# Performance work log

Hardware: AMD Instinct MI355X
Metric: run time of the kernel (lower is better)

Reference implementation:

```python
import jax, jax.numpy as jnp
import numpy as np

B, T, D, H, L = 8, 150, 30, 5, 3
HD = D // H  # 6
ORIG = (300, 74, 35)


def setup_inputs() -> dict:
    key = jax.random.key(0)
    ks = iter(jax.random.split(key, 40))
    def g(shape, s=0.05):
        return jax.random.normal(next(ks), shape, dtype=jnp.float32) * s
    return {
        "x_l": g((B, T, ORIG[0]), 1.0),
        "x_a": g((B, T, ORIG[1]), 1.0),
        "x_v": g((B, T, ORIG[2]), 1.0),
        "Wl": g((D, ORIG[0])),
        "Wa": g((D, ORIG[1])),
        "Wv": g((D, ORIG[2])),
        "in_w": g((2, L, 3 * D, D)),
        "in_b": jnp.zeros((2, L, 3 * D), jnp.float32),
        "out_w": g((2, L, D, D)),
        "out_b": jnp.zeros((2, L, D), jnp.float32),
        "lin1_w": g((2, L, 4 * D, D)),
        "lin1_b": jnp.zeros((2, L, 4 * D), jnp.float32),
        "lin2_w": g((2, L, D, 4 * D)),
        "lin2_b": jnp.zeros((2, L, D), jnp.float32),
        "n1_g": jnp.ones((2, L, D), jnp.float32),
        "n1_b": jnp.zeros((2, L, D), jnp.float32),
        "n2_g": jnp.ones((2, L, D), jnp.float32),
        "n2_b": jnp.zeros((2, L, D), jnp.float32),
        "p1_w": g((2 * D, 2 * D)),
        "p1_b": jnp.zeros((2 * D,), jnp.float32),
        "p2_w": g((2 * D, 2 * D)),
        "p2_b": jnp.zeros((2 * D,), jnp.float32),
        "ow": g((1, 2 * D)),
        "ob": jnp.zeros((1,), jnp.float32),
    }


def _ln(x, g, b, eps=1e-5):
    m = x.mean(-1, keepdims=True)
    v = jnp.var(x, axis=-1, keepdims=True)  # biased var, matches torch LayerNorm
    return (x - m) * jax.lax.rsqrt(v + eps) * g + b


def _heads(x):  # [Tt, B, D] -> [B*H, Tt, HD]
    Tt = x.shape[0]
    return x.reshape(Tt, B * H, HD).transpose(1, 0, 2)


def _layer(x, xk, xv, p):
    iw, ib, ow, ob, w1, b1, w2, b2, g1, bb1, g2, bb2 = p
    res = x
    xn, kn, vn = _ln(x, g1, bb1), _ln(xk, g1, bb1), _ln(xv, g1, bb1)
    q = (xn @ iw[:D].T + ib[:D]) * (HD ** -0.5)
    k = kn @ iw[D:2 * D].T + ib[D:2 * D]
    v = vn @ iw[2 * D:].T + ib[2 * D:]
    qh, kh, vh = _heads(q), _heads(k), _heads(v)
    # trilinear scores: [B*H, Tq, Tk, Tv]
    aw = jnp.einsum('iat,ibt,ict->iabc', qh, kh, vh)
    fused = aw.mean(-1) + aw.max(-1)          # fuse over value axis -> [B*H, Tq, Tk]
    fused = jax.nn.softmax(fused, axis=-1)
    attn = jnp.einsum('iab,ibt->iat', fused, qh)  # NB: original bmm uses q, not v
    attn = attn.transpose(1, 0, 2).reshape(-1, B, D)
    x = res + (attn @ ow.T + ob)
    res = x
    xn = _ln(x, g2, bb2)
    x = jax.nn.relu(xn @ w1.T + b1) @ w2.T + b2
    return res + x


def reference(x_l, x_a, x_v, Wl, Wa, Wv, in_w, in_b, out_w, out_b,
              lin1_w, lin1_b, lin2_w, lin2_b, n1_g, n1_b, n2_g, n2_b,
              p1_w, p1_b, p2_w, p2_b, ow, ob):
    pl = (x_l @ Wl.T).transpose(1, 0, 2)  # [T, B, D] (conv1d k=1, no bias)
    pa = (x_a @ Wa.T).transpose(1, 0, 2)
    pv = (x_v @ Wv.T).transpose(1, 0, 2)
    hs = []
    for s, (kk, vv) in enumerate(((pa, pv), (pv, pa))):
        h = pl
        for l in range(L):
            p = (in_w[s, l], in_b[s, l], out_w[s, l], out_b[s, l],
                 lin1_w[s, l], lin1_b[s, l], lin2_w[s, l], lin2_b[s, l],
                 n1_g[s, l], n1_b[s, l], n2_g[s, l], n2_b[s, l])
            h = _layer(h, kk, vv, p)
        hs.append(h[-1])  # last timestep [B, D]
    last_hs = jnp.concatenate(hs, axis=1)  # [B, 2D]
    proj = jax.nn.relu(last_hs @ p1_w.T + p1_b) @ p2_w.T + p2_b + last_hs
    out = proj @ ow.T + ob
    return (out, last_hs)
```

## Files before the change

kernel.cpp:

```cpp
#include <hip/hip_runtime.h>
#include <math.h>

#define BB 8
#define TT 150
#define DD 30
#define HH 5
#define HD 6
#define LL 3
#define NI 40
#define ROWF (TT*BB*DD)
#define RSTR 8
#define NR 152

typedef _Float16 half8 __attribute__((ext_vector_type(8)));
typedef float f32x16 __attribute__((ext_vector_type(16)));

__device__ __forceinline__ float wsum(float v) {
    #pragma unroll
    for (int m = 32; m > 0; m >>= 1) v += __shfl_xor(v, m, 64);
    return v;
}

__global__ __launch_bounds__(256) void proj3_kernel(
    const float* __restrict__ x_l, const float* __restrict__ x_a, const float* __restrict__ x_v,
    const float* __restrict__ Wl, const float* __restrict__ Wa, const float* __restrict__ Wv,
    float* __restrict__ pl, float* __restrict__ pa, float* __restrict__ pv) {
    int blk = blockIdx.x;
    int which = blk / 300;
    int w = threadIdx.x >> 6, lane = threadIdx.x & 63;
    int rowu = (blk % 300) * 4 + w;
    int t = rowu / BB, b = rowu % BB;
    const float* x = which == 0 ? x_l : (which == 1 ? x_a : x_v);
    const float* W = which == 0 ? Wl : (which == 1 ? Wa : Wv);
    float* out = which == 0 ? pl : (which == 1 ? pa : pv);
    int Cin = which == 0 ? 300 : (which == 1 ? 74 : 35);
    int cst = Cin | 1;
    __shared__ float WS[30 * 301];
    __shared__ float xr[4][304];
    for (int j = threadIdx.x; j < DD * Cin; j += 256)
        WS[(j / Cin) * cst + (j % Cin)] = W[j];
    const float* xp = x + ((size_t)b * TT + t) * Cin;
    for (int j = lane; j < Cin; j += 64) xr[w][j] = xp[j];
    __syncthreads();
    int d = lane >> 1, jh = lane & 1;
    int h1 = Cin >> 1;
    int j0 = jh ? h1 : 0, j1 = jh ? Cin : h1;
    const float* wr = WS + (size_t)(d < DD ? d : 0) * cst;
    float acc = 0.f;
    for (int j = j0; j < j1; j++) acc += xr[w][j] * wr[j];
    acc += __shfl_xor(acc, 1, 64);
    if (jh == 0 && d < DD) out[t * (BB * DD) + b * DD + d] = acc;
}

__global__ __launch_bounds__(256) void kvq0_kernel(
    const float* __restrict__ pl, const float* __restrict__ pa, const float* __restrict__ pv,
    const float* __restrict__ in_w, const float* __restrict__ in_b,
    const float* __restrict__ n1g, const float* __restrict__ n1b,
    _Float16* __restrict__ k_all, _Float16* __restrict__ v_all, _Float16* __restrict__ q) {
    int blk = blockIdx.x;
    int w = threadIdx.x >> 6, lane = threadIdx.x & 63;
    __shared__ float iwS[1800];
    __shared__ float xn[4][2][30];
    if (blk < 1800) {
        int po = blk / 300;
        int s = po / LL;
        int tb = (blk % 300) * 4 + w;
        int t = tb / BB, b = tb % BB;
        const float* xk = (s == 0) ? pa : pv;
        const float* xv = (s == 0) ? pv : pa;
        const float* iw = in_w + (size_t)po * 2700 + 900;
        const float* ib = in_b + (size_t)po * 90;
        const float* g  = n1g + (size_t)po * 30;
        const float* bb = n1b + (size_t)po * 30;
        for (int j = threadIdx.x; j < 1800; j += 256) iwS[j] = iw[j];
        const float* rows[2] = { xk + (size_t)tb * 30, xv + (size_t)tb * 30 };
        for (int r = 0; r < 2; r++) {
            float xval = (lane < 30) ? rows[r][lane] : 0.f;
            float mean = wsum(xval) * (1.f / 30.f);
            float dv = (lane < 30) ? (xval - mean) : 0.f;
            float var = wsum(dv * dv) * (1.f / 30.f);
            float inv = rsqrtf(var + 1e-5f);
            if (lane < 30) xn[w][r][lane] = dv * inv * g[lane] + bb[lane];
        }
        __syncthreads();
        if (lane < 60) {
            int which = lane / 30, dd = lane % 30;
            const float* wr = iwS + lane * 30;
            const float* xv2 = xn[w][which];
            float acc = 0.f;
            #pragma unroll 6
            for (int j = 0; j < 30; j++) acc += wr[j] * xv2[j];
            acc += ib[30 + lane];
            int i = b * HH + dd / HD, hd = dd % HD;
            _Float16* dst = which ? v_all : k_all;
            size_t row = (((size_t)po * NI + i) * TT + t) * 8;
            dst[row + hd] = (_Float16)acc;
            if (hd < 2) dst[row + 6 + hd] = (_Float16)0.f;
        }
    } else {
        int r2 = blk - 1800;
        int s = r2 / 300;
        int tb = (r2 % 300) * 4 + w;
        int t = tb / BB, b = tb % BB;
        int po = s * LL;
        const float* iw = in_w + (size_t)po * 2700;
        const float* ib = in_b + (size_t)po * 90;
        const float* g  = n1g + (size_t)po * 30;
        const float* bb = n1b + (size_t)po * 30;
        for (int j = threadIdx.x; j < 900; j += 256) iwS[j] = iw[j];
        const float* row = pl + (size_t)tb * 30;
        float xval = (lane < 30) ? row[lane] : 0.f;
        float mean = wsum(xval) * (1.f / 30.f);
        float dv = (lane < 30) ? (xval - mean) : 0.f;
        float var = wsum(dv * dv) * (1.f / 30.f);
        float inv = rsqrtf(var + 1e-5f);
        if (lane < 30) xn[w][0][lane] = dv * inv * g[lane] + bb[lane];
        __syncthreads();
        if (lane < 30) {
            const float* wr = iwS + lane * 30;
            float acc = 0.f;
            #pragma unroll 6
            for (int j = 0; j < 30; j++) acc += wr[j] * xn[w][0][j];
            acc = (acc + ib[lane]) * 0.40824829046386307f;
            int i = b * HH + lane / HD, hd = lane % HD;
            size_t rw = (((size_t)s * NI + i) * TT + t) * 8;
            q[rw + hd] = (_Float16)acc;
            if (hd < 2) q[rw + 6 + hd] = (_Float16)0.f;
        }
    }
}

__global__ __launch_bounds__(256, 4) void score_kernel(
    const _Float16* __restrict__ q, const _Float16* __restrict__ k_all,
    const _Float16* __restrict__ v_all, int l, float* __restrict__ attn) {
    int blk = blockIdx.x;
    int s = blk / 760;
    int rem = blk % 760;
    int i = rem / 19;
    int g = rem % 19;
    int tid = threadIdx.x;
    int wv = tid >> 6, lane = tid & 63;
    int lo = lane & 31, hf = lane >> 5;
    int po = s * LL + l;

    __shared__ __align__(16) _Float16 qsh[NR * RSTR];
    __shared__ __align__(16) _Float16 ksh[NR * RSTR];
    __shared__ __align__(16) _Float16 vsh[NR * RSTR];

    const _Float16* qg = q + (size_t)(s * NI + i) * TT * 8;
    const _Float16* kg = k_all + ((size_t)po * NI + i) * TT * 8;
    const _Float16* vg = v_all + ((size_t)po * NI + i) * TT * 8;
    half8 z8;
    #pragma unroll
    for (int t = 0; t < 8; t++) z8[t] = (_Float16)0.f;
    for (int r = tid; r < NR; r += 256) {
        half8 qa = z8, ka = z8, va = z8;
        if (r < TT) {
            qa = *(const half8*)&qg[r * 8];
            ka = *(const half8*)&kg[r * 8];
            va = *(const half8*)&vg[r * 8];
        }
        *(half8*)&qsh[r * RSTR] = qa;
        *(half8*)&ksh[r * RSTR] = ka;
        *(half8*)&vsh[r * RSTR] = va;
    }
    __syncthreads();
    if (wv == 0) {
        float v6[6] = {0.f, 0.f, 0.f, 0.f, 0.f, 0.f};
        for (int c = lane; c < TT; c += 64) {
            #pragma unroll
            for (int t = 0; t < 6; t++) v6[t] += (float)vsh[c * RSTR + t];
        }
        #pragma unroll
        for (int m = 32; m > 0; m >>= 1) {
            #pragma unroll
            for (int t = 0; t < 6; t++) v6[t] += __shfl_xor(v6[t], m, 64);
        }
        if (lane < 6) vsh[TT * RSTR + lane] = (_Float16)(v6[lane] * (1.f / TT));
    }
    __syncthreads();

    f32x16 zacc;
    #pragma unroll
    for (int j = 0; j < 16; j++) zacc[j] = 0.f;

    half8 bfrag[5], vhalf[5];
    #pragma unroll
    for (int nt = 0; nt < 5; nt++) {
        int rr = nt * 32 + lo;
        int rc = rr < 151 ? rr : 151;
        half8 kf = *(const half8*)&ksh[rc * RSTR];
        half8 vf = *(const half8*)&vsh[rc * RSTR];
        bfrag[nt] = hf ? z8 : kf;
        vhalf[nt] = hf ? z8 : vf;
    }

    for (int ap = 0; ap < 2; ap++) {
        int a = g * 8 + wv * 2 + ap;
        if (a >= TT) break;
        half8 qav = *(const half8*)&qsh[a * RSTR];
        half8 afrag[5];
        #pragma unroll
        for (int nt = 0; nt < 5; nt++) afrag[nt] = vhalf[nt] * qav;

        float fsc[5];
        #pragma unroll
        for (int nb = 0; nb < 5; nb++) {
            float tm[4];
            #pragma unroll
            for (int ma = 0; ma < 4; ma++) {
                f32x16 acc = __builtin_amdgcn_mfma_f32_32x32x16_f16(afrag[ma], bfrag[nb], zacc, 0, 0, 0);
                float p0 = fmaxf(acc[0], acc[1]);
                float p1 = fmaxf(acc[2], acc[3]);
                float p2 = fmaxf(acc[4], acc[5]);
                float p3 = fmaxf(acc[6], acc[7]);
                float p4 = fmaxf(acc[8], acc[9]);
                float p5 = fmaxf(acc[10], acc[11]);
                float p6 = fmaxf(acc[12], acc[13]);
                float p7 = fmaxf(acc[14], acc[15]);
                float q0 = fmaxf(p0, p1), q1 = fmaxf(p2, p3);
                float q2 = fmaxf(p4, p5), q3 = fmaxf(p6, p7);
                tm[ma] = fmaxf(fmaxf(q0, q1), fmaxf(q2, q3));
            }
            f32x16 a4 = __builtin_amdgcn_mfma_f32_32x32x16_f16(afrag[4], bfrag[nb], zacc, 0, 0, 0);
            float s0 = fmaxf(a4[0], a4[1]);
            float s1 = fmaxf(a4[2], a4[3]);
            float s2 = fmaxf(a4[4], a4[5]);
            float s3 = fmaxf(a4[6], a4[7]);
            float s4 = fmaxf(a4[8], a4[9]);
            float ext = (hf == 0) ? fmaxf(a4[10], a4[11]) : -INFINITY;
            float m4 = fmaxf(fmaxf(fmaxf(s0, s1), fmaxf(s2, s3)), fmaxf(s4, ext));
            float rm = fmaxf(fmaxf(fmaxf(tm[0], tm[1]), fmaxf(tm[2], tm[3])), m4);
            float om = __shfl_xor(a4[10], 32, 64);
            float mn = hf ? a4[10] : om;
            rm = fmaxf(rm, __shfl_xor(rm, 32, 64));
            int bcol = nb * 32 + lo;
            fsc[nb] = (bcol < TT) ? (mn + rm) : -INFINITY;
        }
        float m = fmaxf(fmaxf(fsc[0], fsc[1]), fmaxf(fsc[2], fmaxf(fsc[3], fsc[4])));
        #pragma unroll
        for (int msk = 16; msk > 0; msk >>= 1) m = fmaxf(m, __shfl_xor(m, msk, 64));
        float e[5], es = 0.f;
        #pragma unroll
        for (int nb = 0; nb < 5; nb++) { e[nb] = __expf(fsc[nb] - m); es += e[nb]; }
        #pragma unroll
        for (int msk = 16; msk > 0; msk >>= 1) es += __shfl_xor(es, msk, 64);
        float acc6[6] = {0.f, 0.f, 0.f, 0.f, 0.f, 0.f};
        #pragma unroll
        for (int nb = 0; nb < 5; nb++) {
            int bcol = nb * 32 + lo;
            int bi = (bcol < TT) ? bcol : 0;
            float wgt = e[nb];
            half8 qrow = *(const half8*)&qsh[bi * RSTR];
            #pragma unroll
            for (int t = 0; t < 6; t++) acc6[t] += wgt * (float)qrow[t];
        }
        #pragma unroll
        for (int msk = 16; msk > 0; msk >>= 1) {
            #pragma unroll
            for (int t = 0; t < 6; t++) acc6[t] += __shfl_xor(acc6[t], msk, 64);
        }
        if (lane == 0) {
            float inv = 1.f / es;
            int bo = i / HH, ho = i % HH;
            float* dst = attn + (size_t)s * ROWF + a * (BB * DD) + bo * DD + ho * HD;
            #pragma unroll
            for (int t = 0; t < 6; t++) dst[t] = acc6[t] * inv;
        }
    }
}

__global__ __launch_bounds__(256) void ffnlnq_kernel(
    const float* __restrict__ attn, const float* __restrict__ pl,
    const float* __restrict__ out_w, const float* __restrict__ out_b,
    const float* __restrict__ l1w, const float* __restrict__ l1b,
    const float* __restrict__ l2w, const float* __restrict__ l2b,
    const float* __restrict__ n2g, const float* __restrict__ n2b,
    const float* __restrict__ in_w, const float* __restrict__ in_b,
    const float* __restrict__ n1g, const float* __restrict__ n1b,
    int l, int has_next,
    float* __restrict__ h, _Float16* __restrict__ q) {
    int blk = blockIdx.x;
    int s = blk / 300;
    int w = threadIdx.x >> 6, lane = threadIdx.x & 63;
    int tb = (blk % 300) * 4 + w;
    int t = tb / BB, b = tb % BB;
    int po = s * LL + l;
    const float* ow = out_w + (size_t)po * 900;
    const float* ob = out_b + (size_t)po * 30;
    const float* w1 = l1w + (size_t)po * 3600;
    const float* b1 = l1b + (size_t)po * 120;
    const float* w2 = l2w + (size_t)po * 3600;
    const float* b2 = l2b + (size_t)po * 30;
    const float* g2 = n2g + (size_t)po * 30;
    const float* bb2 = n2b + (size_t)po * 30;
    __shared__ float owS[900];
    __shared__ float w1T[30 * 128];
    __shared__ float w2S[30 * 121];
    __shared__ float iwqS[900];
    __shared__ float arS[4][30], xnS[4][32], hidS[4][120], xqS[4][30];
    for (int j = threadIdx.x; j < 900; j += 256) owS[j] = ow[j];
    for (int j = threadIdx.x; j < 3600; j += 256) w1T[(j % 30) * 128 + (j / 30)] = w1[j];
    for (int j = threadIdx.x; j < 3600; j += 256) w2S[(j / 120) * 121 + (j % 120)] = w2[j];
    if (has_next) {
        const float* iwq = in_w + (size_t)(po + 1) * 2700;
        for (int j = threadIdx.x; j < 900; j += 256) iwqS[j] = iwq[j];
    }
    __syncthreads();
    float* hrow = h + (size_t)s * ROWF + (size_t)tb * 30;
    const float* res = (l == 0) ? (pl + (size_t)tb * 30) : hrow;
    const float* arow = attn + (size_t)s * ROWF + (size_t)tb * 30;
    if (lane < 30) arS[w][lane] = arow[lane];
    float x1v = 0.f;
    if (lane < 30) {
        const float* wr = owS + lane * 30;
        float acc = 0.f;
        #pragma unroll 6
        for (int j = 0; j < 30; j++) acc += wr[j] * arS[w][j];
        x1v = res[lane] + acc + ob[lane];
    }
    float mean = wsum(x1v) * (1.f / 30.f);
    float dv = (lane < 30) ? (x1v - mean) : 0.f;
    float var = wsum(dv * dv) * (1.f / 30.f);
    float inv = rsqrtf(var + 1e-5f);
    if (lane < 30) xnS[w][lane] = dv * inv * g2[lane] + bb2[lane];
    for (int o = lane; o < 120; o += 64) {
        float acc = 0.f;
        #pragma unroll 6
        for (int j = 0; j < 30; j++) acc += w1T[j * 128 + o] * xnS[w][j];
        hidS[w][o] = fmaxf(acc + b1[o], 0.f);
    }
    float newh = 0.f;
    if (lane < 30) {
        const float* wr = w2S + lane * 121;
        float acc = 0.f;
        #pragma unroll 8
        for (int j = 0; j < 120; j++) acc += wr[j] * hidS[w][j];
        newh = x1v + acc + b2[lane];
        hrow[lane] = newh;
    }
    if (has_next) {
        const float* g1 = n1g + (size_t)(po + 1) * 30;
        const float* bb1 = n1b + (size_t)(po + 1) * 30;
        const float* ibq = in_b + (size_t)(po + 1) * 90;
        float mean2 = wsum(newh) * (1.f / 30.f);
        float dv2 = (lane < 30) ? (newh - mean2) : 0.f;
        float var2 = wsum(dv2 * dv2) * (1.f / 30.f);
        float inv2 = rsqrtf(var2 + 1e-5f);
        if (lane < 30) xqS[w][lane] = dv2 * inv2 * g1[lane] + bb1[lane];
        if (lane < 30) {
            const float* wr = iwqS + lane * 30;
            float acc = 0.f;
            #pragma unroll 6
            for (int j = 0; j < 30; j++) acc += wr[j] * xqS[w][j];
            acc = (acc + ibq[lane]) * 0.40824829046386307f;
            int i = b * HH + lane / HD, hd = lane % HD;
            size_t rw = (((size_t)s * NI + i) * TT + t) * 8;
            q[rw + hd] = (_Float16)acc;
            if (hd < 2) q[rw + 6 + hd] = (_Float16)0.f;
        }
    }
}

__global__ __launch_bounds__(256) void head_kernel(
    const float* __restrict__ h,
    const float* __restrict__ p1w, const float* __restrict__ p1b,
    const float* __restrict__ p2w, const float* __restrict__ p2b,
    const float* __restrict__ ow, const float* __restrict__ ob,
    float* __restrict__ out) {
    int tid = threadIdx.x;
    __shared__ float lh[480], hid[480], pr[480];
    for (int idx = tid; idx < 480; idx += 256) {
        int b = idx / 60, j = idx % 60;
        int s = j / 30, d = j % 30;
        float vv = h[(size_t)s * ROWF + 149 * (BB * DD) + b * DD + d];
        lh[idx] = vv;
        out[8 + idx] = vv;
    }
    __syncthreads();
    for (int idx = tid; idx < 480; idx += 256) {
        int b = idx / 60, o = idx % 60;
        const float* wr = p1w + o * 60;
        float acc = p1b[o];
        for (int j = 0; j < 60; j++) acc += wr[j] * lh[b * 60 + j];
        hid[idx] = fmaxf(acc, 0.f);
    }
    __syncthreads();
    for (int idx = tid; idx < 480; idx += 256) {
        int b = idx / 60, d = idx % 60;
        const float* wr = p2w + d * 60;
        float acc = p2b[d];
        for (int j = 0; j < 60; j++) acc += wr[j] * hid[b * 60 + j];
        pr[idx] = acc + lh[idx];
    }
    __syncthreads();
    if (tid < 8) {
        float acc = ob[0];
        for (int j = 0; j < 60; j++) acc += pr[tid * 60 + j] * ow[j];
        out[tid] = acc;
    }
}

extern "C" void kernel_launch(void* const* d_in, const int* in_sizes, int n_in,
                              void* d_out, int out_size, void* d_ws, size_t ws_size,
                              hipStream_t stream) {
    const float* x_l   = (const float*)d_in[0];
    const float* x_a   = (const float*)d_in[1];
    const float* x_v   = (const float*)d_in[2];
    const float* Wl    = (const float*)d_in[3];
    const float* Wa    = (const float*)d_in[4];
    const float* Wv    = (const float*)d_in[5];
    const float* in_w  = (const float*)d_in[6];
    const float* in_b  = (const float*)d_in[7];
    const float* out_w = (const float*)d_in[8];
    const float* out_b = (const float*)d_in[9];
    const float* l1w   = (const float*)d_in[10];
    const float* l1b   = (const float*)d_in[11];
    const float* l2w   = (const float*)d_in[12];
    const float* l2b   = (const float*)d_in[13];
    const float* n1g   = (const float*)d_in[14];
    const float* n1b   = (const float*)d_in[15];
    const float* n2g   = (const float*)d_in[16];
    const float* n2b   = (const float*)d_in[17];
    const float* p1w   = (const float*)d_in[18];
    const float* p1b   = (const float*)d_in[19];
    const float* p2w   = (const float*)d_in[20];
    const float* p2b   = (const float*)d_in[21];
    const float* oww   = (const float*)d_in[22];
    const float* obb   = (const float*)d_in[23];

    float* ws = (float*)d_ws;
    float* pl    = ws;
    float* pa    = ws + 36000;
    float* pv    = ws + 72000;
    float* h     = ws + 108000;
    float* at    = ws + 180000;
    _Float16* qh = (_Float16*)(ws + 252000);
    _Float16* kh = (_Float16*)(ws + 300000);
    _Float16* vh = (_Float16*)(ws + 444000);

    proj3_kernel<<<900, 256, 0, stream>>>(x_l, x_a, x_v, Wl, Wa, Wv, pl, pa, pv);
    kvq0_kernel<<<2400, 256, 0, stream>>>(pl, pa, pv, in_w, in_b, n1g, n1b,
                                          kh, vh, qh);
    for (int l = 0; l < LL; l++) {
        score_kernel<<<1520, 256, 0, stream>>>(qh, kh, vh, l, at);
        ffnlnq_kernel<<<600, 256, 0, stream>>>(at, pl, out_w, out_b, l1w, l1b, l2w, l2b,
                                               n2g, n2b, in_w, in_b, n1g, n1b,
                                               l, (l < LL - 1) ? 1 : 0, h, qh);
    }
    head_kernel<<<1, 256, 0, stream>>>(h, p1w, p1b, p2w, p2b, oww, obb, (float*)d_out);
}
```

Baseline: 247.9 us.

## Fuse input projection with K/V/Q prep and give score blocks more query rows

Merges the three modality projections and the layer-0 K/V/Q LayerNorm+projection into one kernel. Each (t,b) row is projected once, its normalization statistics are computed once and reused across all six parameter sets, and the pa/pv intermediate buffers are removed. Weights are now read straight from global memory instead of being staged in shared memory. Separately, the score kernel has each wave handle four query rows instead of two, halving the grid so the K/V staging is amortized over more work, at the cost of fewer blocks and less parallelism.

```diff
diff --git a/kernel.cpp b/kernel.cpp
--- a/kernel.cpp
+++ b/kernel.cpp
@@ -21,112 +21,126 @@
     return v;
 }
 
-__global__ __launch_bounds__(256) void proj3_kernel(
+__global__ __launch_bounds__(256) void projkvq_kernel(
     const float* __restrict__ x_l, const float* __restrict__ x_a, const float* __restrict__ x_v,
     const float* __restrict__ Wl, const float* __restrict__ Wa, const float* __restrict__ Wv,
-    float* __restrict__ pl, float* __restrict__ pa, float* __restrict__ pv) {
-    int blk = blockIdx.x;
-    int which = blk / 300;
-    int w = threadIdx.x >> 6, lane = threadIdx.x & 63;
-    int rowu = (blk % 300) * 4 + w;
-    int t = rowu / BB, b = rowu % BB;
-    const float* x = which == 0 ? x_l : (which == 1 ? x_a : x_v);
-    const float* W = which == 0 ? Wl : (which == 1 ? Wa : Wv);
-    float* out = which == 0 ? pl : (which == 1 ? pa : pv);
-    int Cin = which == 0 ? 300 : (which == 1 ? 74 : 35);
-    int cst = Cin | 1;
-    __shared__ float WS[30 * 301];
-    __shared__ float xr[4][304];
-    for (int j = threadIdx.x; j < DD * Cin; j += 256)
-        WS[(j / Cin) * cst + (j % Cin)] = W[j];
-    const float* xp = x + ((size_t)b * TT + t) * Cin;
-    for (int j = lane; j < Cin; j += 64) xr[w][j] = xp[j];
-    __syncthreads();
-    int d = lane >> 1, jh = lane & 1;
-    int h1 = Cin >> 1;
-    int j0 = jh ? h1 : 0, j1 = jh ? Cin : h1;
-    const float* wr = WS + (size_t)(d < DD ? d : 0) * cst;
-    float acc = 0.f;
-    for (int j = j0; j < j1; j++) acc += xr[w][j] * wr[j];
-    acc += __shfl_xor(acc, 1, 64);
-    if (jh == 0 && d < DD) out[t * (BB * DD) + b * DD + d] = acc;
-}
-
-__global__ __launch_bounds__(256) void kvq0_kernel(
-    const float* __restrict__ pl, const float* __restrict__ pa, const float* __restrict__ pv,
     const float* __restrict__ in_w, const float* __restrict__ in_b,
     const float* __restrict__ n1g, const float* __restrict__ n1b,
+    float* __restrict__ pl,
     _Float16* __restrict__ k_all, _Float16* __restrict__ v_all, _Float16* __restrict__ q) {
     int blk = blockIdx.x;
     int w = threadIdx.x >> 6, lane = threadIdx.x & 63;
-    __shared__ float iwS[1800];
-    __shared__ float xn[4][2][30];
-    if (blk < 1800) {
-        int po = blk / 300;
+    int tb = blk * 4 + w;
+    int t = tb / BB, b = tb % BB;
+
+    __shared__ float xl[4][304];
+    __shared__ float xa[4][80];
+    __shared__ float xv[4][40];
+    __shared__ float rrow[3][4][32];
+    __shared__ float dco[4][3][32];
+    __shared__ float xkv[4][2][32];
+    __shared__ float xq[4][32];
+
+    const float* xpl = x_l + ((size_t)b * TT + t) * 300;
+    const float* xpa = x_a + ((size_t)b * TT + t) * 74;
+    const float* xpv = x_v + ((size_t)b * TT + t) * 35;
+    for (int j = lane; j < 300; j += 64) xl[w][j] = xpl[j];
+    for (int j = lane; j < 74; j += 64) xa[w][j] = xpa[j];
+    if (lane < 35) xv[w][lane] = xpv[lane];
+    __syncthreads();
+
+    int d = lane >> 1, jh = lane & 1;
+    int dc = d < DD ? d : 0;
+    float accL, accA, accV;
+    {
+        const float* wr = Wl + (size_t)dc * 300;
+        int j0 = jh ? 150 : 0, j1 = jh ? 300 : 150;
+        float acc = 0.f;
+        for (int j = j0; j < j1; j++) acc += xl[w][j] * wr[j];
+        acc += __shfl_xor(acc, 1, 64);
+        accL = acc;
+    }
+    {
+        const float* wr = Wa + (size_t)dc * 74;
+        int j0 = jh ? 37 : 0, j1 = jh ? 74 : 37;
+        float acc = 0.f;
+        for (int j = j0; j < j1; j++) acc += xa[w][j] * wr[j];
+        acc += __shfl_xor(acc, 1, 64);
+        accA = acc;
+    }
+    {
+        const float* wr = Wv + (size_t)dc * 35;
+        int j0 = jh ? 17 : 0, j1 = jh ? 35 : 17;
+        float acc = 0.f;
+        for (int j = j0; j < j1; j++) acc += xv[w][j] * wr[j];
+        acc += __shfl_xor(acc, 1, 64);
+        accV = acc;
+    }
+    if (jh == 0 && d < DD) {
+        pl[t * (BB * DD) + b * DD + d] = accL;
+        rrow[0][w][d] = accL;
+        rrow[1][w][d] = accA;
+        rrow[2][w][d] = accV;
+    }
+    __syncthreads();
+
+    #pragma unroll
+    for (int src = 0; src < 3; src++) {
+        float xval = (lane < 30) ? rrow[src][w][lane] : 0.f;
+        float mean = wsum(xval) * (1.f / 30.f);
+        float dv = (lane < 30) ? (xval - mean) : 0.f;
+        float var = wsum(dv * dv) * (1.f / 30.f);
+        float inv = rsqrtf(var + 1e-5f);
+        if (lane < 30) dco[w][src][lane] = dv * inv;
+    }
+    __syncthreads();
+
+    for (int po = 0; po < 6; po++) {
         int s = po / LL;
-        int tb = (blk % 300) * 4 + w;
-        int t = tb / BB, b = tb % BB;
-        const float* xk = (s == 0) ? pa : pv;
-        const float* xv = (s == 0) ? pv : pa;
-        const float* iw = in_w + (size_t)po * 2700 + 900;
-        const float* ib = in_b + (size_t)po * 90;
-        const float* g  = n1g + (size_t)po * 30;
+        int kin = (s == 0) ? 1 : 2;
+        int vin = (s == 0) ? 2 : 1;
+        const float* g = n1g + (size_t)po * 30;
         const float* bb = n1b + (size_t)po * 30;
-        for (int j = threadIdx.x; j < 1800; j += 256) iwS[j] = iw[j];
-        const float* rows[2] = { xk + (size_t)tb * 30, xv + (size_t)tb * 30 };
-        for (int r = 0; r < 2; r++) {
-            float xval = (lane < 30) ? rows[r][lane] : 0.f;
-            float mean = wsum(xval) * (1.f / 30.f);
-            float dv = (lane < 30) ? (xval - mean) : 0.f;
-            float var = wsum(dv * dv) * (1.f / 30.f);
-            float inv = rsqrtf(var + 1e-5f);
-            if (lane < 30) xn[w][r][lane] = dv * inv * g[lane] + bb[lane];
+        int half = lane >> 5, dd2 = lane & 31;
+        if (dd2 < 30) {
+            int sel = half ? vin : kin;
+            xkv[w][half][dd2] = dco[w][sel][dd2] * g[dd2] + bb[dd2];
         }
         __syncthreads();
         if (lane < 60) {
             int which = lane / 30, dd = lane % 30;
-            const float* wr = iwS + lane * 30;
-            const float* xv2 = xn[w][which];
+            const float* wr = in_w + (size_t)po * 2700 + 900 + lane * 30;
             float acc = 0.f;
             #pragma unroll 6
-            for (int j = 0; j < 30; j++) acc += wr[j] * xv2[j];
-            acc += ib[30 + lane];
+            for (int j = 0; j < 30; j++) acc += wr[j] * xkv[w][which][j];
+            acc += in_b[po * 90 + 30 + lane];
             int i = b * HH + dd / HD, hd = dd % HD;
             _Float16* dst = which ? v_all : k_all;
             size_t row = (((size_t)po * NI + i) * TT + t) * 8;
             dst[row + hd] = (_Float16)acc;
             if (hd < 2) dst[row + 6 + hd] = (_Float16)0.f;
         }
-    } else {
-        int r2 = blk - 1800;
-        int s = r2 / 300;
-        int tb = (r2 % 300) * 4 + w;
-        int t = tb / BB, b = tb % BB;
-        int po = s * LL;
-        const float* iw = in_w + (size_t)po * 2700;
-        const float* ib = in_b + (size_t)po * 90;
-        const float* g  = n1g + (size_t)po * 30;
+        __syncthreads();
+    }
+
+    for (int s2 = 0; s2 < 2; s2++) {
+        int po = s2 * LL;
+        const float* g = n1g + (size_t)po * 30;
         const float* bb = n1b + (size_t)po * 30;
-        for (int j = threadIdx.x; j < 900; j += 256) iwS[j] = iw[j];
-        const float* row = pl + (size_t)tb * 30;
-        float xval = (lane < 30) ? row[lane] : 0.f;
-        float mean = wsum(xval) * (1.f / 30.f);
-        float dv = (lane < 30) ? (xval - mean) : 0.f;
-        float var = wsum(dv * dv) * (1.f / 30.f);
-        float inv = rsqrtf(var + 1e-5f);
-        if (lane < 30) xn[w][0][lane] = dv * inv * g[lane] + bb[lane];
+        if (lane < 30) xq[w][lane] = dco[w][0][lane] * g[lane] + bb[lane];
         __syncthreads();
         if (lane < 30) {
-            const float* wr = iwS + lane * 30;
+            const float* wr = in_w + (size_t)po * 2700 + lane * 30;
             float acc = 0.f;
             #pragma unroll 6
-            for (int j = 0; j < 30; j++) acc += wr[j] * xn[w][0][j];
-            acc = (acc + ib[lane]) * 0.40824829046386307f;
+            for (int j = 0; j < 30; j++) acc += wr[j] * xq[w][j];
+            acc = (acc + in_b[po * 90 + lane]) * 0.40824829046386307f;
             int i = b * HH + lane / HD, hd = lane % HD;
-            size_t rw = (((size_t)s * NI + i) * TT + t) * 8;
+            size_t rw = (((size_t)s2 * NI + i) * TT + t) * 8;
             q[rw + hd] = (_Float16)acc;
             if (hd < 2) q[rw + 6 + hd] = (_Float16)0.f;
         }
+        __syncthreads();
     }
 }
 
@@ -134,10 +148,10 @@
     const _Float16* __restrict__ q, const _Float16* __restrict__ k_all,
     const _Float16* __restrict__ v_all, int l, float* __restrict__ attn) {
     int blk = blockIdx.x;
-    int s = blk / 760;
-    int rem = blk % 760;
-    int i = rem / 19;
-    int g = rem % 19;
+    int s = blk / 400;
+    int rem = blk % 400;
+    int i = rem / 10;
+    int g2 = rem % 10;
     int tid = threadIdx.x;
     int wv = tid >> 6, lane = tid & 63;
     int lo = lane & 31, hf = lane >> 5;
@@ -195,8 +209,8 @@
         vhalf[nt] = hf ? z8 : vf;
     }
 
-    for (int ap = 0; ap < 2; ap++) {
-        int a = g * 8 + wv * 2 + ap;
+    for (int ap = 0; ap < 4; ap++) {
+        int a = g2 * 16 + wv * 4 + ap;
         if (a >= TT) break;
         half8 qav = *(const half8*)&qsh[a * RSTR];
         half8 afrag[5];
@@ -431,19 +445,17 @@
 
     float* ws = (float*)d_ws;
     float* pl    = ws;
-    float* pa    = ws + 36000;
-    float* pv    = ws + 72000;
-    float* h     = ws + 108000;
-    float* at    = ws + 180000;
-    _Float16* qh = (_Float16*)(ws + 252000);
-    _Float16* kh = (_Float16*)(ws + 300000);
-    _Float16* vh = (_Float16*)(ws + 444000);
-
-    proj3_kernel<<<900, 256, 0, stream>>>(x_l, x_a, x_v, Wl, Wa, Wv, pl, pa, pv);
-    kvq0_kernel<<<2400, 256, 0, stream>>>(pl, pa, pv, in_w, in_b, n1g, n1b,
-                                          kh, vh, qh);
+    float* h     = ws + 36000;
+    float* at    = ws + 108000;
+    _Float16* qh = (_Float16*)(ws + 180000);
+    _Float16* kh = (_Float16*)(ws + 228000);
+    _Float16* vh = (_Float16*)(ws + 372000);
+
+    projkvq_kernel<<<300, 256, 0, stream>>>(x_l, x_a, x_v, Wl, Wa, Wv,
+                                            in_w, in_b, n1g, n1b,
+                                            pl, kh, vh, qh);
     for (int l = 0; l < LL; l++) {
-        score_kernel<<<1520, 256, 0, stream>>>(qh, kh, vh, l, at);
+        score_kernel<<<800, 256, 0, stream>>>(qh, kh, vh, l, at);
         ffnlnq_kernel<<<600, 256, 0, stream>>>(at, pl, out_w, out_b, l1w, l1b, l2w, l2b,
                                                n2g, n2b, in_w, in_b, n1g, n1b,
                                                l, (l < LL - 1) ? 1 : 0, h, qh);
```

Result: slower. 293.5 us (+18.4%).
